# Kernel optimization log

Measured on AMD Instinct MI355X. Metric: run time of the kernel, lower is better.

Reference implementation:

```python
import jax, jax.numpy as jnp
import numpy as np

N = 50000      # nodes
E = 800000     # edges (avg degree 16)
DIN = 128
DOUT = 64
ALPHA = 0.5    # DirGATConv mixing coefficient
NEG_SLOPE = 0.2  # PyG GATConv default negative_slope


def setup_inputs() -> dict:
    key = jax.random.key(0)
    ks = jax.random.split(key, 12)
    x = jax.random.normal(ks[0], (N, DIN), jnp.float32)
    edge_index = jax.random.randint(ks[1], (2, E), 0, N, dtype=jnp.int64)

    def p(k, shape):
        return jax.random.normal(k, shape, jnp.float32) * 0.05

    return dict(
        x=x,
        edge_index=edge_index,
        W1=p(ks[2], (DIN, DOUT)), att_src1=p(ks[3], (DOUT,)), att_dst1=p(ks[4], (DOUT,)), b1=jnp.zeros((DOUT,), jnp.float32),
        W2=p(ks[5], (DIN, DOUT)), att_src2=p(ks[6], (DOUT,)), att_dst2=p(ks[7], (DOUT,)), b2=jnp.zeros((DOUT,), jnp.float32),
    )


def _gat_conv(x, src, dst, W, a_src, a_dst, b):
    """PyG GATConv with heads=1: linear, per-dst softmax attention, scatter-add."""
    n = x.shape[0]
    loops = jnp.arange(n, dtype=src.dtype)
    src = jnp.concatenate([src, loops])  # add_self_loops=True (PyG default)
    dst = jnp.concatenate([dst, loops])

    xw = x @ W                                # [N, DOUT]
    a_s = xw @ a_src                          # [N]  per-node src attention score
    a_d = xw @ a_dst                          # [N]  per-node dst attention score
    e = jax.nn.leaky_relu(a_s[src] + a_d[dst], NEG_SLOPE)  # [E+N]

    # numerically-stable softmax over edges grouped by destination node
    m = jax.ops.segment_max(e, dst, num_segments=n)
    m = jnp.where(jnp.isfinite(m), m, 0.0)    # nodes w/o in-edges -> safe value
    ex = jnp.exp(e - m[dst])
    denom = jax.ops.segment_sum(ex, dst, num_segments=n)
    coef = ex / (denom[dst] + 1e-16)          # [E+N]

    out = jax.ops.segment_sum(coef[:, None] * xw[src], dst, num_segments=n)
    return out + b


def reference(x, edge_index, W1, att_src1, att_dst1, b1, W2, att_src2, att_dst2, b2):
    src, dst = edge_index[0], edge_index[1]
    out_fwd = _gat_conv(x, src, dst, W1, att_src1, att_dst1, b1)   # src -> dst
    out_rev = _gat_conv(x, dst, src, W2, att_src2, att_dst2, b2)   # dst -> src (transposed edges)
    return (1.0 - ALPHA) * out_fwd + ALPHA * out_rev
```

## Files before the change

### kernel.cpp

```cpp
#include <hip/hip_runtime.h>

#define DIN 128
#define DOUT 64
#define NEG_SLOPE 0.2f
#define ALPHA 0.5f
#define NBUK 512
#define EPB  4096

typedef __attribute__((ext_vector_type(8))) short bf16x8;
typedef __attribute__((ext_vector_type(4))) float f32x4;

__device__ __forceinline__ float lrelu(float x) { return x > 0.0f ? x : NEG_SLOPE * x; }

__device__ __forceinline__ unsigned short f2bf(float f) {
    unsigned u = __float_as_uint(f);
    unsigned r = (u + 0x7fffu + ((u >> 16) & 1u)) >> 16;
    return (unsigned short)r;
}
__device__ __forceinline__ float bf2f(unsigned short h) {
    return __uint_as_float((unsigned)h << 16);
}
__device__ __forceinline__ float readlane_f(float v, int l) {
    return __int_as_float(__builtin_amdgcn_readlane(__float_as_int(v), l));
}

__global__ __launch_bounds__(64) void wfrag_kernel(
    const float* __restrict__ W1, const float* __restrict__ W2,
    unsigned short* __restrict__ wf)
{
    int combo = blockIdx.x;
    int mat = combo >> 4;
    int kk = (combo >> 2) & 3;
    int t = combo & 3;
    int l = threadIdx.x;
    int g = l >> 4, c = l & 15;
    const float* W = mat ? W2 : W1;
    #pragma unroll
    for (int j = 0; j < 8; ++j) {
        float w = W[(kk * 32 + g * 8 + j) * DOUT + t * 16 + c];
        unsigned short hi = f2bf(w);
        unsigned short lo = f2bf(w - bf2f(hi));
        wf[(size_t)(((mat * 2 + 0) * 16 + kk * 4 + t) * 512) + l * 8 + j] = hi;
        wf[(size_t)(((mat * 2 + 1) * 16 + kk * 4 + t) * 512) + l * 8 + j] = lo;
    }
}

__global__ __launch_bounds__(256) void proj_kernel(
    const float* __restrict__ x, const unsigned short* __restrict__ wf,
    const float* __restrict__ as1, const float* __restrict__ ad1,
    const float* __restrict__ as2, const float* __restrict__ ad2,
    unsigned short* __restrict__ xw1, unsigned short* __restrict__ xw2,
    float* __restrict__ s1, float* __restrict__ d1,
    float* __restrict__ s2, float* __restrict__ d2, int n)
{
    int ntiles = (n + 15) >> 4;
    int tile = blockIdx.x * 4 + (threadIdx.x >> 6);
    if (tile >= ntiles) return;
    int l = threadIdx.x & 63;
    int g = l >> 4, c = l & 15;

    int arow = tile * 16 + c;
    if (arow >= n) arow = n - 1;

    bf16x8 ahi[4], alo[4];
    const float* xr = x + (size_t)arow * DIN + g * 8;
    #pragma unroll
    for (int kk = 0; kk < 4; ++kk) {
        float4 v0 = *(const float4*)(xr + kk * 32);
        float4 v1 = *(const float4*)(xr + kk * 32 + 4);
        float xv[8] = {v0.x, v0.y, v0.z, v0.w, v1.x, v1.y, v1.z, v1.w};
        #pragma unroll
        for (int j = 0; j < 8; ++j) {
            unsigned short hi = f2bf(xv[j]);
            unsigned short lo = f2bf(xv[j] - bf2f(hi));
            ahi[kk][j] = (short)hi;
            alo[kk][j] = (short)lo;
        }
    }

    float vs1[4] = {0, 0, 0, 0}, vd1[4] = {0, 0, 0, 0};
    float vs2[4] = {0, 0, 0, 0}, vd2[4] = {0, 0, 0, 0};
    const bf16x8* wfv = (const bf16x8*)wf;

    #pragma unroll
    for (int t = 0; t < 4; ++t) {
        f32x4 C1 = {0.f, 0.f, 0.f, 0.f}, C2 = {0.f, 0.f, 0.f, 0.f};
        #pragma unroll
        for (int kk = 0; kk < 4; ++kk) {
            bf16x8 bh1 = wfv[(size_t)((0 * 16 + kk * 4 + t) * 64) + l];
            bf16x8 bl1 = wfv[(size_t)((1 * 16 + kk * 4 + t) * 64) + l];
            bf16x8 bh2 = wfv[(size_t)((2 * 16 + kk * 4 + t) * 64) + l];
            bf16x8 bl2 = wfv[(size_t)((3 * 16 + kk * 4 + t) * 64) + l];
            C1 = __builtin_amdgcn_mfma_f32_16x16x32_bf16(ahi[kk], bh1, C1, 0, 0, 0);
            C1 = __builtin_amdgcn_mfma_f32_16x16x32_bf16(alo[kk], bh1, C1, 0, 0, 0);
            C1 = __builtin_amdgcn_mfma_f32_16x16x32_bf16(ahi[kk], bl1, C1, 0, 0, 0);
            C2 = __builtin_amdgcn_mfma_f32_16x16x32_bf16(ahi[kk], bh2, C2, 0, 0, 0);
            C2 = __builtin_amdgcn_mfma_f32_16x16x32_bf16(alo[kk], bh2, C2, 0, 0, 0);
            C2 = __builtin_amdgcn_mfma_f32_16x16x32_bf16(ahi[kk], bl2, C2, 0, 0, 0);
        }
        float a1v = as1[t * 16 + c], a2v = ad1[t * 16 + c];
        float a3v = as2[t * 16 + c], a4v = ad2[t * 16 + c];
        #pragma unroll
        for (int r = 0; r < 4; ++r) {
            vs1[r] = fmaf(C1[r], a1v, vs1[r]);
            vd1[r] = fmaf(C1[r], a2v, vd1[r]);
            vs2[r] = fmaf(C2[r], a3v, vs2[r]);
            vd2[r] = fmaf(C2[r], a4v, vd2[r]);
        }
        #pragma unroll
        for (int r = 0; r < 4; ++r) {
            int node = tile * 16 + g * 4 + r;
            if (node < n) {
                xw1[(size_t)node * DOUT + t * 16 + c] = f2bf(C1[r]);
                xw2[(size_t)node * DOUT + t * 16 + c] = f2bf(C2[r]);
            }
        }
    }
    #pragma unroll
    for (int off = 1; off < 16; off <<= 1) {
        #pragma unroll
        for (int r = 0; r < 4; ++r) {
            vs1[r] += __shfl_xor(vs1[r], off);
            vd1[r] += __shfl_xor(vd1[r], off);
            vs2[r] += __shfl_xor(vs2[r], off);
            vd2[r] += __shfl_xor(vd2[r], off);
        }
    }
    if (c == 0) {
        #pragma unroll
        for (int r = 0; r < 4; ++r) {
            int node = tile * 16 + g * 4 + r;
            if (node < n) {
                s1[node] = vs1[r]; d1[node] = vd1[r];
                s2[node] = vs2[r]; d2[node] = vd2[r];
            }
        }
    }
}

__global__ __launch_bounds__(256) void binhist_kernel(
    const int* __restrict__ src, const int* __restrict__ dst,
    int* __restrict__ hist, int e, int n, int nblk)
{
    __shared__ int cnt[NBUK];
    int tid = threadIdx.x, blk = blockIdx.x;
    for (int b = tid; b < NBUK; b += 256) cnt[b] = 0;
    __syncthreads();
    int base = blk * EPB;
    for (int k = 0; k < EPB / 256; ++k) {
        int t = base + k * 256 + tid;
        if (t < e) {
            int s = src[t], d = dst[t];
            atomicAdd(&cnt[d >> 8], 1);
            atomicAdd(&cnt[(n + s) >> 8], 1);
        }
    }
    __syncthreads();
    for (int b = tid; b < NBUK; b += 256)
        hist[(size_t)b * nblk + blk] = cnt[b];
}

__global__ __launch_bounds__(256) void scan_part_kernel(
    const int* __restrict__ deg, int* __restrict__ part, int n2)
{
    __shared__ int sm[256];
    int b = blockIdx.x, t = threadIdx.x;
    int base = b * 1024 + t * 4;
    int s = 0;
    #pragma unroll
    for (int k = 0; k < 4; ++k) { int i = base + k; if (i < n2) s += deg[i]; }
    sm[t] = s; __syncthreads();
    for (int o = 128; o; o >>= 1) { if (t < o) sm[t] += sm[t + o]; __syncthreads(); }
    if (t == 0) part[b] = sm[0];
}

__global__ __launch_bounds__(1024) void scan_mid_kernel(
    int* __restrict__ part, int nb, int* __restrict__ offs, int n2, int total)
{
    __shared__ int sm[1024];
    int t = threadIdx.x;
    int v = (t < nb) ? part[t] : 0;
    sm[t] = v; __syncthreads();
    for (int o = 1; o < 1024; o <<= 1) {
        int u = (t >= o) ? sm[t - o] : 0;
        __syncthreads();
        sm[t] += u;
        __syncthreads();
    }
    if (t < nb) part[t] = sm[t] - v;
    if (t == 0) offs[n2] = total;
}

__global__ __launch_bounds__(256) void scan_apply_kernel(
    const int* __restrict__ deg, const int* __restrict__ part,
    int* __restrict__ offs, int n2)
{
    __shared__ int sm[256];
    int b = blockIdx.x, t = threadIdx.x;
    int base = b * 1024 + t * 4;
    int d[4]; int s = 0;
    #pragma unroll
    for (int k = 0; k < 4; ++k) { int i = base + k; d[k] = (i < n2) ? deg[i] : 0; s += d[k]; }
    sm[t] = s; __syncthreads();
    for (int o = 1; o < 256; o <<= 1) {
        int u = (t >= o) ? sm[t - o] : 0;
        __syncthreads();
        sm[t] += u;
        __syncthreads();
    }
    int run = part[b] + sm[t] - s;
    #pragma unroll
    for (int k = 0; k < 4; ++k) {
        int i = base + k;
        if (i < n2) { offs[i] = run; run += d[k]; }
    }
}

__global__ __launch_bounds__(256) void binscatter_kernel(
    const int* __restrict__ src, const int* __restrict__ dst,
    const int* __restrict__ hscan, unsigned* __restrict__ staging,
    int e, int n, int nblk)
{
    __shared__ int cur[NBUK];
    int tid = threadIdx.x, blk = blockIdx.x;
    for (int b = tid; b < NBUK; b += 256)
        cur[b] = hscan[(size_t)b * nblk + blk];
    __syncthreads();
    int base = blk * EPB;
    for (int k = 0; k < EPB / 256; ++k) {
        int t = base + k * 256 + tid;
        if (t < e) {
            int s = src[t], d = dst[t];
            int pF = atomicAdd(&cur[d >> 8], 1);
            staging[pF] = ((unsigned)(d & 255) << 16) | (unsigned)s;
            int segR = n + s;
            int pR = atomicAdd(&cur[segR >> 8], 1);
            staging[pR] = ((unsigned)(segR & 255) << 16) | (unsigned)d;
        }
    }
}

__global__ __launch_bounds__(256) void buildcsr_kernel(
    const int* __restrict__ hscan, const unsigned* __restrict__ staging,
    int* __restrict__ csr, int* __restrict__ offs,
    int n2, int e2, int nblk)
{
    __shared__ int segcnt[256];
    __shared__ int segoff[256];
    int b = blockIdx.x, tid = threadIdx.x;
    int lo = hscan[(size_t)b * nblk];
    int hi = hscan[(size_t)(b + 1) * nblk];
    segcnt[tid] = 0;
    __syncthreads();
    for (int idx = lo + tid; idx < hi; idx += 256)
        atomicAdd(&segcnt[staging[idx] >> 16], 1);
    __syncthreads();
    if (tid < 64) {
        int a0 = segcnt[4 * tid], a1 = segcnt[4 * tid + 1];
        int a2 = segcnt[4 * tid + 2], a3 = segcnt[4 * tid + 3];
        int s = a0 + a1 + a2 + a3;
        int inc = s;
        #pragma unroll
        for (int off = 1; off < 64; off <<= 1) {
            int u = __shfl_up(inc, off);
            if (tid >= off) inc += u;
        }
        int excl = inc - s;
        segoff[4 * tid] = excl;
        segoff[4 * tid + 1] = excl + a0;
        segoff[4 * tid + 2] = excl + a0 + a1;
        segoff[4 * tid + 3] = excl + a0 + a1 + a2;
    }
    __syncthreads();
    {
        int seg = (b << 8) + tid;
        if (seg < n2) offs[seg] = lo + segoff[tid];
        segcnt[tid] = segoff[tid];
    }
    if (b == gridDim.x - 1 && tid == 0) offs[n2] = e2;
    __syncthreads();
    for (int idx = lo + tid; idx < hi; idx += 256) {
        unsigned st = staging[idx];
        int pos = atomicAdd(&segcnt[st >> 16], 1);
        csr[lo + pos] = (int)(st & 0xFFFFu);
    }
}

__global__ __launch_bounds__(256) void gather_kernel(
    const int* __restrict__ offs, const int* __restrict__ csr,
    const float* __restrict__ s1, const float* __restrict__ d1,
    const float* __restrict__ s2, const float* __restrict__ d2,
    const unsigned short* __restrict__ xw1, const unsigned short* __restrict__ xw2,
    const float* __restrict__ b1, const float* __restrict__ b2,
    float* __restrict__ out, int n)
{
    int i = (blockIdx.x * 256 + threadIdx.x) >> 6;
    int lane = threadIdx.x & 63;
    if (i >= n) return;

    float d1i = d1[i], d2i = d2[i];
    int cF = offs[i],     endF = offs[i + 1];
    int cR = offs[n + i], endR = offs[n + i + 1];

    float pSF = __expf(lrelu(s1[i] + d1i));
    float pSR = __expf(lrelu(s2[i] + d2i));
    float lF = pSF, lR = pSR;
    float aF0 = pSF * bf2f(xw1[(size_t)i * DOUT + lane]), aF1 = 0.f, aF2 = 0.f, aF3 = 0.f;
    float aR0 = pSR * bf2f(xw2[(size_t)i * DOUT + lane]), aR1 = 0.f, aR2 = 0.f, aR3 = 0.f;

    while (cF < endF || cR < endR) {
        int cntF = endF - cF; cntF = cntF < 0 ? 0 : (cntF > 64 ? 64 : cntF);
        int cntR = endR - cR; cntR = cntR < 0 ? 0 : (cntR > 64 ? 64 : cntR);

        int jF = 0, jR = 0;
        float pF = 0.0f, pR = 0.0f;
        if (lane < cntF) { jF = csr[cF + lane]; pF = __expf(lrelu(s1[jF] + d1i)); }
        if (lane < cntR) { jR = csr[cR + lane]; pR = __expf(lrelu(s2[jR] + d2i)); }

        float psF = pF, psR = pR;
        #pragma unroll
        for (int off = 32; off; off >>= 1) {
            psF += __shfl_xor(psF, off);
            psR += __shfl_xor(psR, off);
        }
        lF += psF;
        lR += psR;

        int tmax = cntF > cntR ? cntF : cntR;
        int t = 0;
        for (; t + 4 <= tmax; t += 4) {
            float pF0 = readlane_f(pF, t),     pF1 = readlane_f(pF, t + 1);
            float pF2 = readlane_f(pF, t + 2), pF3 = readlane_f(pF, t + 3);
            int   jF0 = __builtin_amdgcn_readlane(jF, t);
            int   jF1 = __builtin_amdgcn_readlane(jF, t + 1);
            int   jF2 = __builtin_amdgcn_readlane(jF, t + 2);
            int   jF3 = __builtin_amdgcn_readlane(jF, t + 3);
            float pR0 = readlane_f(pR, t),     pR1 = readlane_f(pR, t + 1);
            float pR2 = readlane_f(pR, t + 2), pR3 = readlane_f(pR, t + 3);
            int   jR0 = __builtin_amdgcn_readlane(jR, t);
            int   jR1 = __builtin_amdgcn_readlane(jR, t + 1);
            int   jR2 = __builtin_amdgcn_readlane(jR, t + 2);
            int   jR3 = __builtin_amdgcn_readlane(jR, t + 3);
            aF0 = fmaf(pF0, bf2f(xw1[(size_t)jF0 * DOUT + lane]), aF0);
            aF1 = fmaf(pF1, bf2f(xw1[(size_t)jF1 * DOUT + lane]), aF1);
            aF2 = fmaf(pF2, bf2f(xw1[(size_t)jF2 * DOUT + lane]), aF2);
            aF3 = fmaf(pF3, bf2f(xw1[(size_t)jF3 * DOUT + lane]), aF3);
            aR0 = fmaf(pR0, bf2f(xw2[(size_t)jR0 * DOUT + lane]), aR0);
            aR1 = fmaf(pR1, bf2f(xw2[(size_t)jR1 * DOUT + lane]), aR1);
            aR2 = fmaf(pR2, bf2f(xw2[(size_t)jR2 * DOUT + lane]), aR2);
            aR3 = fmaf(pR3, bf2f(xw2[(size_t)jR3 * DOUT + lane]), aR3);
        }
        for (; t < tmax; ++t) {
            float pF0 = readlane_f(pF, t);
            int   jF0 = __builtin_amdgcn_readlane(jF, t);
            float pR0 = readlane_f(pR, t);
            int   jR0 = __builtin_amdgcn_readlane(jR, t);
            aF0 = fmaf(pF0, bf2f(xw1[(size_t)jF0 * DOUT + lane]), aF0);
            aR0 = fmaf(pR0, bf2f(xw2[(size_t)jR0 * DOUT + lane]), aR0);
        }
        cF += cntF;
        cR += cntR;
    }

    float resF = ((aF0 + aF1) + (aF2 + aF3)) / (lF + 1e-16f);
    float resR = ((aR0 + aR1) + (aR2 + aR3)) / (lR + 1e-16f);
    out[(size_t)i * DOUT + lane] =
        (1.0f - ALPHA) * (resF + b1[lane]) + ALPHA * (resR + b2[lane]);
}

extern "C" void kernel_launch(void* const* d_in, const int* in_sizes, int n_in,
                              void* d_out, int out_size, void* d_ws, size_t ws_size,
                              hipStream_t stream) {
    const float* x   = (const float*)d_in[0];
    const int*   ei  = (const int*)d_in[1];
    const float* W1  = (const float*)d_in[2];
    const float* as1 = (const float*)d_in[3];
    const float* ad1 = (const float*)d_in[4];
    const float* b1  = (const float*)d_in[5];
    const float* W2  = (const float*)d_in[6];
    const float* as2 = (const float*)d_in[7];
    const float* ad2 = (const float*)d_in[8];
    const float* b2  = (const float*)d_in[9];
    float* out = (float*)d_out;

    int n = in_sizes[0] / DIN;
    int e = in_sizes[1] / 2;
    const int* src = ei;
    const int* dst = ei + e;
    int n2 = 2 * n;
    int e2 = 2 * e;
    int nblk = (e + EPB - 1) / EPB;
    int L = NBUK * nblk;
    int ntile = (L + 1023) / 1024;
    int nbuk_eff = (n2 + 255) >> 8;
    int ntiles16 = (n + 15) >> 4;

    unsigned short* xw1 = (unsigned short*)d_ws;
    unsigned short* xw2 = xw1 + (size_t)n * DOUT;
    float* s1  = (float*)(xw2 + (size_t)n * DOUT);
    float* d1  = s1 + n;
    float* s2  = d1 + n;
    float* d2  = s2 + n;
    unsigned short* wf = (unsigned short*)(d2 + n);
    int* hist  = (int*)(wf + 32768);
    int* hscan = hist + (size_t)L;
    int* part  = hscan + (size_t)L + 1;
    int* offs  = part + 1024;
    int* csr   = offs + (size_t)n2 + 1;
    unsigned* staging = (unsigned*)(csr + (size_t)e2);

    wfrag_kernel<<<32, 64, 0, stream>>>(W1, W2, wf);
    proj_kernel<<<(ntiles16 + 3) / 4, 256, 0, stream>>>(x, wf, as1, ad1, as2, ad2,
                                                        xw1, xw2, s1, d1, s2, d2, n);

    binhist_kernel<<<nblk, 256, 0, stream>>>(src, dst, hist, e, n, nblk);
    scan_part_kernel<<<ntile, 256, 0, stream>>>(hist, part, L);
    scan_mid_kernel<<<1, 1024, 0, stream>>>(part, ntile, hscan, L, e2);
    scan_apply_kernel<<<ntile, 256, 0, stream>>>(hist, part, hscan, L);
    binscatter_kernel<<<nblk, 256, 0, stream>>>(src, dst, hscan, staging, e, n, nblk);
    buildcsr_kernel<<<nbuk_eff, 256, 0, stream>>>(hscan, staging, csr, offs, n2, e2, nblk);

    long long gthreads = (long long)n * 64;
    int gblocks = (int)((gthreads + 255) / 256);
    gather_kernel<<<gblocks, 256, 0, stream>>>(offs, csr, s1, d1, s2, d2,
                                               xw1, xw2, b1, b2, out, n);
}
```

Before: 115.5 us.

## Fuse CSR build stages with projection blocks and cache staging in LDS

Merges the weight-fragment prep, histogram, three scan stages and bin-scatter into five kernels, each also running a slice of the projection GEMM blocks. This cuts kernel launches and lets the compute-heavy projection overlap the latency-bound scan stages. Separately, buildcsr now caches its staging slice in shared memory so the second pass reads LDS instead of global memory, with a global fallback when the slice exceeds the cache. The costs are more LDS per block in buildcsr, which may lower occupancy, and a scan_mid stage shrunk to 256 threads, which assumes at most 256 scan tiles.

```diff
diff --git a/kernel.cpp b/kernel.cpp
--- a/kernel.cpp
+++ b/kernel.cpp
@@ -6,6 +6,7 @@
 #define ALPHA 0.5f
 #define NBUK 512
 #define EPB  4096
+#define BCCAP 6144
 
 typedef __attribute__((ext_vector_type(8))) short bf16x8;
 typedef __attribute__((ext_vector_type(4))) float f32x4;
@@ -24,15 +25,16 @@
     return __int_as_float(__builtin_amdgcn_readlane(__float_as_int(v), l));
 }
 
-__global__ __launch_bounds__(64) void wfrag_kernel(
+
+__device__ __forceinline__ void dev_wfrag(
     const float* __restrict__ W1, const float* __restrict__ W2,
-    unsigned short* __restrict__ wf)
-{
-    int combo = blockIdx.x;
+    unsigned short* __restrict__ wf, int blk, int tid)
+{
+    int combo = blk * 4 + (tid >> 6);
     int mat = combo >> 4;
     int kk = (combo >> 2) & 3;
     int t = combo & 3;
-    int l = threadIdx.x;
+    int l = tid & 63;
     int g = l >> 4, c = l & 15;
     const float* W = mat ? W2 : W1;
     #pragma unroll
@@ -45,18 +47,111 @@
     }
 }
 
-__global__ __launch_bounds__(256) void proj_kernel(
+__device__ __forceinline__ void dev_binhist(
+    const int* __restrict__ src, const int* __restrict__ dst,
+    int* __restrict__ hist, int e, int n, int nblk, int blk, int tid, int* cnt)
+{
+    for (int b = tid; b < NBUK; b += 256) cnt[b] = 0;
+    __syncthreads();
+    int base = blk * EPB;
+    for (int k = 0; k < EPB / 256; ++k) {
+        int t = base + k * 256 + tid;
+        if (t < e) {
+            int s = src[t], d = dst[t];
+            atomicAdd(&cnt[d >> 8], 1);
+            atomicAdd(&cnt[(n + s) >> 8], 1);
+        }
+    }
+    __syncthreads();
+    for (int b = tid; b < NBUK; b += 256)
+        hist[(size_t)b * nblk + blk] = cnt[b];
+}
+
+__device__ __forceinline__ void dev_scan_part(
+    const int* __restrict__ deg, int* __restrict__ part, int L, int blk, int tid, int* sm)
+{
+    int base = blk * 1024 + tid * 4;
+    int s = 0;
+    #pragma unroll
+    for (int k = 0; k < 4; ++k) { int i = base + k; if (i < L) s += deg[i]; }
+    sm[tid] = s; __syncthreads();
+    for (int o = 128; o; o >>= 1) { if (tid < o) sm[tid] += sm[tid + o]; __syncthreads(); }
+    if (tid == 0) part[blk] = sm[0];
+}
+
+__device__ __forceinline__ void dev_scan_mid(
+    int* __restrict__ part, int nb, int* __restrict__ hscan, int L, int total,
+    int tid, int* sm)
+{
+    int v = (tid < nb) ? part[tid] : 0;
+    sm[tid] = v; __syncthreads();
+    for (int o = 1; o < 256; o <<= 1) {
+        int u = (tid >= o) ? sm[tid - o] : 0;
+        __syncthreads();
+        sm[tid] += u;
+        __syncthreads();
+    }
+    if (tid < nb) part[tid] = sm[tid] - v;
+    if (tid == 0) hscan[L] = total;
+}
+
+__device__ __forceinline__ void dev_scan_apply(
+    const int* __restrict__ deg, const int* __restrict__ part,
+    int* __restrict__ hscan, int L, int blk, int tid, int* sm)
+{
+    int base = blk * 1024 + tid * 4;
+    int d[4]; int s = 0;
+    #pragma unroll
+    for (int k = 0; k < 4; ++k) { int i = base + k; d[k] = (i < L) ? deg[i] : 0; s += d[k]; }
+    sm[tid] = s; __syncthreads();
+    for (int o = 1; o < 256; o <<= 1) {
+        int u = (tid >= o) ? sm[tid - o] : 0;
+        __syncthreads();
+        sm[tid] += u;
+        __syncthreads();
+    }
+    int run = part[blk] + sm[tid] - s;
+    #pragma unroll
+    for (int k = 0; k < 4; ++k) {
+        int i = base + k;
+        if (i < L) { hscan[i] = run; run += d[k]; }
+    }
+}
+
+__device__ __forceinline__ void dev_binscatter(
+    const int* __restrict__ src, const int* __restrict__ dst,
+    const int* __restrict__ hscan, unsigned* __restrict__ staging,
+    int e, int n, int nblk, int blk, int tid, int* cur)
+{
+    for (int b = tid; b < NBUK; b += 256)
+        cur[b] = hscan[(size_t)b * nblk + blk];
+    __syncthreads();
+    int base = blk * EPB;
+    for (int k = 0; k < EPB / 256; ++k) {
+        int t = base + k * 256 + tid;
+        if (t < e) {
+            int s = src[t], d = dst[t];
+            int pF = atomicAdd(&cur[d >> 8], 1);
+            staging[pF] = ((unsigned)(d & 255) << 16) | (unsigned)s;
+            int segR = n + s;
+            int pR = atomicAdd(&cur[segR >> 8], 1);
+            staging[pR] = ((unsigned)(segR & 255) << 16) | (unsigned)d;
+        }
+    }
+}
+
+__device__ __forceinline__ void dev_proj(
     const float* __restrict__ x, const unsigned short* __restrict__ wf,
     const float* __restrict__ as1, const float* __restrict__ ad1,
     const float* __restrict__ as2, const float* __restrict__ ad2,
     unsigned short* __restrict__ xw1, unsigned short* __restrict__ xw2,
     float* __restrict__ s1, float* __restrict__ d1,
-    float* __restrict__ s2, float* __restrict__ d2, int n)
+    float* __restrict__ s2, float* __restrict__ d2, int n, int projblk, int tid)
 {
     int ntiles = (n + 15) >> 4;
-    int tile = blockIdx.x * 4 + (threadIdx.x >> 6);
+    int tile = projblk * 4 + (tid >> 6);
     if (tile >= ntiles) return;
-    int l = threadIdx.x & 63;
+    int l = tid & 63;
     int g = l >> 4, c = l & 15;
 
     int arow = tile * 16 + c;
@@ -138,106 +233,84 @@
     }
 }
 
-__global__ __launch_bounds__(256) void binhist_kernel(
+
+__global__ __launch_bounds__(256) void fused1_kernel(
+    const float* __restrict__ W1, const float* __restrict__ W2,
+    unsigned short* __restrict__ wf,
     const int* __restrict__ src, const int* __restrict__ dst,
     int* __restrict__ hist, int e, int n, int nblk)
 {
-    __shared__ int cnt[NBUK];
-    int tid = threadIdx.x, blk = blockIdx.x;
-    for (int b = tid; b < NBUK; b += 256) cnt[b] = 0;
-    __syncthreads();
-    int base = blk * EPB;
-    for (int k = 0; k < EPB / 256; ++k) {
-        int t = base + k * 256 + tid;
-        if (t < e) {
-            int s = src[t], d = dst[t];
-            atomicAdd(&cnt[d >> 8], 1);
-            atomicAdd(&cnt[(n + s) >> 8], 1);
-        }
-    }
-    __syncthreads();
-    for (int b = tid; b < NBUK; b += 256)
-        hist[(size_t)b * nblk + blk] = cnt[b];
-}
-
-__global__ __launch_bounds__(256) void scan_part_kernel(
-    const int* __restrict__ deg, int* __restrict__ part, int n2)
-{
-    __shared__ int sm[256];
-    int b = blockIdx.x, t = threadIdx.x;
-    int base = b * 1024 + t * 4;
-    int s = 0;
-    #pragma unroll
-    for (int k = 0; k < 4; ++k) { int i = base + k; if (i < n2) s += deg[i]; }
-    sm[t] = s; __syncthreads();
-    for (int o = 128; o; o >>= 1) { if (t < o) sm[t] += sm[t + o]; __syncthreads(); }
-    if (t == 0) part[b] = sm[0];
-}
-
-__global__ __launch_bounds__(1024) void scan_mid_kernel(
-    int* __restrict__ part, int nb, int* __restrict__ offs, int n2, int total)
-{
-    __shared__ int sm[1024];
-    int t = threadIdx.x;
-    int v = (t < nb) ? part[t] : 0;
-    sm[t] = v; __syncthreads();
-    for (int o = 1; o < 1024; o <<= 1) {
-        int u = (t >= o) ? sm[t - o] : 0;
-        __syncthreads();
-        sm[t] += u;
-        __syncthreads();
-    }
-    if (t < nb) part[t] = sm[t] - v;
-    if (t == 0) offs[n2] = total;
-}
-
-__global__ __launch_bounds__(256) void scan_apply_kernel(
-    const int* __restrict__ deg, const int* __restrict__ part,
-    int* __restrict__ offs, int n2)
-{
-    __shared__ int sm[256];
-    int b = blockIdx.x, t = threadIdx.x;
-    int base = b * 1024 + t * 4;
-    int d[4]; int s = 0;
-    #pragma unroll
-    for (int k = 0; k < 4; ++k) { int i = base + k; d[k] = (i < n2) ? deg[i] : 0; s += d[k]; }
-    sm[t] = s; __syncthreads();
-    for (int o = 1; o < 256; o <<= 1) {
-        int u = (t >= o) ? sm[t - o] : 0;
-        __syncthreads();
-        sm[t] += u;
-        __syncthreads();
-    }
-    int run = part[b] + sm[t] - s;
-    #pragma unroll
-    for (int k = 0; k < 4; ++k) {
-        int i = base + k;
-        if (i < n2) { offs[i] = run; run += d[k]; }
-    }
-}
-
-__global__ __launch_bounds__(256) void binscatter_kernel(
+    __shared__ int smem[NBUK];
+    int blk = blockIdx.x, tid = threadIdx.x;
+    if (blk < 8) dev_wfrag(W1, W2, wf, blk, tid);
+    else dev_binhist(src, dst, hist, e, n, nblk, blk - 8, tid, smem);
+}
+
+__global__ __launch_bounds__(256) void fused2_kernel(
+    const int* __restrict__ hist, int* __restrict__ part, int L, int ntile,
+    const float* __restrict__ x, const unsigned short* __restrict__ wf,
+    const float* __restrict__ as1, const float* __restrict__ ad1,
+    const float* __restrict__ as2, const float* __restrict__ ad2,
+    unsigned short* __restrict__ xw1, unsigned short* __restrict__ xw2,
+    float* __restrict__ s1, float* __restrict__ d1,
+    float* __restrict__ s2, float* __restrict__ d2, int n, int proj0)
+{
+    __shared__ int smem[256];
+    int blk = blockIdx.x, tid = threadIdx.x;
+    if (blk < ntile) dev_scan_part(hist, part, L, blk, tid, smem);
+    else dev_proj(x, wf, as1, ad1, as2, ad2, xw1, xw2, s1, d1, s2, d2, n,
+                  proj0 + blk - ntile, tid);
+}
+
+__global__ __launch_bounds__(256) void fused3_kernel(
+    int* __restrict__ part, int ntile, int* __restrict__ hscan, int L, int total,
+    const float* __restrict__ x, const unsigned short* __restrict__ wf,
+    const float* __restrict__ as1, const float* __restrict__ ad1,
+    const float* __restrict__ as2, const float* __restrict__ ad2,
+    unsigned short* __restrict__ xw1, unsigned short* __restrict__ xw2,
+    float* __restrict__ s1, float* __restrict__ d1,
+    float* __restrict__ s2, float* __restrict__ d2, int n, int proj0)
+{
+    __shared__ int smem[256];
+    int blk = blockIdx.x, tid = threadIdx.x;
+    if (blk == 0) dev_scan_mid(part, ntile, hscan, L, total, tid, smem);
+    else dev_proj(x, wf, as1, ad1, as2, ad2, xw1, xw2, s1, d1, s2, d2, n,
+                  proj0 + blk - 1, tid);
+}
+
+__global__ __launch_bounds__(256) void fused4_kernel(
+    const int* __restrict__ hist, const int* __restrict__ part,
+    int* __restrict__ hscan, int L, int ntile,
+    const float* __restrict__ x, const unsigned short* __restrict__ wf,
+    const float* __restrict__ as1, const float* __restrict__ ad1,
+    const float* __restrict__ as2, const float* __restrict__ ad2,
+    unsigned short* __restrict__ xw1, unsigned short* __restrict__ xw2,
+    float* __restrict__ s1, float* __restrict__ d1,
+    float* __restrict__ s2, float* __restrict__ d2, int n, int proj0)
+{
+    __shared__ int smem[256];
+    int blk = blockIdx.x, tid = threadIdx.x;
+    if (blk < ntile) dev_scan_apply(hist, part, hscan, L, blk, tid, smem);
+    else dev_proj(x, wf, as1, ad1, as2, ad2, xw1, xw2, s1, d1, s2, d2, n,
+                  proj0 + blk - ntile, tid);
+}
+
+__global__ __launch_bounds__(256) void fused5_kernel(
     const int* __restrict__ src, const int* __restrict__ dst,
     const int* __restrict__ hscan, unsigned* __restrict__ staging,
-    int e, int n, int nblk)
-{
-    __shared__ int cur[NBUK];
-    int tid = threadIdx.x, blk = blockIdx.x;
-    for (int b = tid; b < NBUK; b += 256)
-        cur[b] = hscan[(size_t)b * nblk + blk];
-    __syncthreads();
-    int base = blk * EPB;
-    for (int k = 0; k < EPB / 256; ++k) {
-        int t = base + k * 256 + tid;
-        if (t < e) {
-            int s = src[t], d = dst[t];
-            int pF = atomicAdd(&cur[d >> 8], 1);
-            staging[pF] = ((unsigned)(d & 255) << 16) | (unsigned)s;
-            int segR = n + s;
-            int pR = atomicAdd(&cur[segR >> 8], 1);
-            staging[pR] = ((unsigned)(segR & 255) << 16) | (unsigned)d;
-        }
-    }
+    int e, int nblk,
+    const float* __restrict__ x, const unsigned short* __restrict__ wf,
+    const float* __restrict__ as1, const float* __restrict__ ad1,
+    const float* __restrict__ as2, const float* __restrict__ ad2,
+    unsigned short* __restrict__ xw1, unsigned short* __restrict__ xw2,
+    float* __restrict__ s1, float* __restrict__ d1,
+    float* __restrict__ s2, float* __restrict__ d2, int n, int proj0)
+{
+    __shared__ int smem[NBUK];
+    int blk = blockIdx.x, tid = threadIdx.x;
+    if (blk < nblk) dev_binscatter(src, dst, hscan, staging, e, n, nblk, blk, tid, smem);
+    else dev_proj(x, wf, as1, ad1, as2, ad2, xw1, xw2, s1, d1, s2, d2, n,
+                  proj0 + blk - nblk, tid);
 }
 
 __global__ __launch_bounds__(256) void buildcsr_kernel(
@@ -247,13 +320,23 @@
 {
     __shared__ int segcnt[256];
     __shared__ int segoff[256];
+    __shared__ unsigned cache[BCCAP];
     int b = blockIdx.x, tid = threadIdx.x;
     int lo = hscan[(size_t)b * nblk];
     int hi = hscan[(size_t)(b + 1) * nblk];
+    int span = hi - lo;
     segcnt[tid] = 0;
     __syncthreads();
-    for (int idx = lo + tid; idx < hi; idx += 256)
-        atomicAdd(&segcnt[staging[idx] >> 16], 1);
+    if (span <= BCCAP) {
+        for (int k = tid; k < span; k += 256) {
+            unsigned st = staging[lo + k];
+            cache[k] = st;
+            atomicAdd(&segcnt[st >> 16], 1);
+        }
+    } else {
+        for (int idx = lo + tid; idx < hi; idx += 256)
+            atomicAdd(&segcnt[staging[idx] >> 16], 1);
+    }
     __syncthreads();
     if (tid < 64) {
         int a0 = segcnt[4 * tid], a1 = segcnt[4 * tid + 1];
@@ -279,10 +362,18 @@
     }
     if (b == gridDim.x - 1 && tid == 0) offs[n2] = e2;
     __syncthreads();
-    for (int idx = lo + tid; idx < hi; idx += 256) {
-        unsigned st = staging[idx];
-        int pos = atomicAdd(&segcnt[st >> 16], 1);
-        csr[lo + pos] = (int)(st & 0xFFFFu);
+    if (span <= BCCAP) {
+        for (int k = tid; k < span; k += 256) {
+            unsigned st = cache[k];
+            int pos = atomicAdd(&segcnt[st >> 16], 1);
+            csr[lo + pos] = (int)(st & 0xFFFFu);
+        }
+    } else {
+        for (int idx = lo + tid; idx < hi; idx += 256) {
+            unsigned st = staging[idx];
+            int pos = atomicAdd(&segcnt[st >> 16], 1);
+            csr[lo + pos] = (int)(st & 0xFFFFu);
+        }
     }
 }
 
@@ -394,6 +485,10 @@
     int ntile = (L + 1023) / 1024;
     int nbuk_eff = (n2 + 255) >> 8;
     int ntiles16 = (n + 15) >> 4;
+    int projblks = (ntiles16 + 3) / 4;
+
+    int pc0 = projblks / 4, pc1 = projblks / 4, pc2 = projblks / 4;
+    int pc3 = projblks - pc0 - pc1 - pc2;
 
     unsigned short* xw1 = (unsigned short*)d_ws;
     unsigned short* xw2 = xw1 + (size_t)n * DOUT;
@@ -409,15 +504,20 @@
     int* csr   = offs + (size_t)n2 + 1;
     unsigned* staging = (unsigned*)(csr + (size_t)e2);
 
-    wfrag_kernel<<<32, 64, 0, stream>>>(W1, W2, wf);
-    proj_kernel<<<(ntiles16 + 3) / 4, 256, 0, stream>>>(x, wf, as1, ad1, as2, ad2,
-                                                        xw1, xw2, s1, d1, s2, d2, n);
-
-    binhist_kernel<<<nblk, 256, 0, stream>>>(src, dst, hist, e, n, nblk);
-    scan_part_kernel<<<ntile, 256, 0, stream>>>(hist, part, L);
-    scan_mid_kernel<<<1, 1024, 0, stream>>>(part, ntile, hscan, L, e2);
-    scan_apply_kernel<<<ntile, 256, 0, stream>>>(hist, part, hscan, L);
-    binscatter_kernel<<<nblk, 256, 0, stream>>>(src, dst, hscan, staging, e, n, nblk);
+    fused1_kernel<<<8 + nblk, 256, 0, stream>>>(W1, W2, wf, src, dst, hist, e, n, nblk);
+
+    fused2_kernel<<<ntile + pc0, 256, 0, stream>>>(hist, part, L, ntile,
+        x, wf, as1, ad1, as2, ad2, xw1, xw2, s1, d1, s2, d2, n, 0);
+
+    fused3_kernel<<<1 + pc1, 256, 0, stream>>>(part, ntile, hscan, L, e2,
+        x, wf, as1, ad1, as2, ad2, xw1, xw2, s1, d1, s2, d2, n, pc0);
+
+    fused4_kernel<<<ntile + pc2, 256, 0, stream>>>(hist, part, hscan, L, ntile,
+        x, wf, as1, ad1, as2, ad2, xw1, xw2, s1, d1, s2, d2, n, pc0 + pc1);
+
+    fused5_kernel<<<nblk + pc3, 256, 0, stream>>>(src, dst, hscan, staging, e, nblk,
+        x, wf, as1, ad1, as2, ad2, xw1, xw2, s1, d1, s2, d2, n, pc0 + pc1 + pc2);
+
     buildcsr_kernel<<<nbuk_eff, 256, 0, stream>>>(hscan, staging, csr, offs, n2, e2, nblk);
 
     long long gthreads = (long long)n * 64;
```

Result: faster. 113.1 us (-2.1%).
